# Kernel tuning notes

Hardware: AMD Instinct MI355X
Metric: run time of the kernel (lower is better)

The kernel has to match this reference:

```python
import jax, jax.numpy as jnp
import numpy as np

N_NODES = 100000
N_EDGES = 800000
# (in_dim, out_channels_per_head, heads) for the 5 stacked GATConv layers
DIMS = [(32, 24, 10), (240, 24, 5), (120, 24, 2), (48, 24, 1), (24, 12, 1)]
NEG_SLOPE = 0.2  # PyG GATConv default leaky_relu slope


def setup_inputs() -> dict:
    key = jax.random.key(0)
    ks = jax.random.split(key, 4 + 4 * len(DIMS))
    x = jax.random.normal(ks[0], (N_NODES, 32), jnp.float32)
    # edge_index with no self loops (dst = src + nonzero offset mod N),
    # since PyG GATConv removes then re-adds self loops.
    src = jax.random.randint(ks[1], (N_EDGES,), 0, N_NODES)
    off = jax.random.randint(ks[2], (N_EDGES,), 1, N_NODES)
    dst = (src + off) % N_NODES
    edge_index = jnp.stack([src, dst]).astype(jnp.int32)
    edge_attr = jax.random.normal(ks[3], (N_EDGES, 4), jnp.float32)
    inp = {"x": x, "edge_index": edge_index, "edge_attr": edge_attr}
    for i, (din, c, h) in enumerate(DIMS):
        kw, kb, ka, kd = ks[4 + 4 * i: 8 + 4 * i]
        s = 1.0 / np.sqrt(din)
        inp[f"W{i}"] = jax.random.normal(kw, (din, h * c), jnp.float32) * s
        inp[f"b{i}"] = jax.random.normal(kb, (h * c,), jnp.float32) * 0.01
        inp[f"as{i}"] = jax.random.normal(ka, (h, c), jnp.float32) * (1.0 / np.sqrt(c))
        inp[f"ad{i}"] = jax.random.normal(kd, (h, c), jnp.float32) * (1.0 / np.sqrt(c))
    return inp


def gat_layer(x, src, dst, W, b, a_src, a_dst):
    # Faithful PyG GATConv (concat=True, bias=True, edge_dim=None)
    n = x.shape[0]
    h_heads, c = a_src.shape
    h = (x @ W).reshape(n, h_heads, c)                      # [N,H,C]
    alpha_s = jnp.einsum('nhc,hc->nh', h, a_src)            # [N,H]
    alpha_d = jnp.einsum('nhc,hc->nh', h, a_dst)            # [N,H]
    e = jax.nn.leaky_relu(alpha_s[src] + alpha_d[dst], NEG_SLOPE)  # [E,H]
    # segment softmax over incoming edges of each destination node
    m = jax.ops.segment_max(e, dst, num_segments=n)         # [N,H]
    ex = jnp.exp(e - m[dst])
    z = jax.ops.segment_sum(ex, dst, num_segments=n)        # [N,H]
    attn = ex / z[dst]                                      # [E,H]
    out = jax.ops.segment_sum(h[src] * attn[:, :, None], dst, num_segments=n)
    return out.reshape(n, h_heads * c) + b


def reference(x, edge_index, edge_attr,
              W0, b0, as0, ad0, W1, b1, as1, ad1, W2, b2, as2, ad2,
              W3, b3, as3, ad3, W4, b4, as4, ad4):
    # edge_attr is ignored: GATConv(edge_dim=None) does not use it.
    n = x.shape[0]
    loop = jnp.arange(n, dtype=edge_index.dtype)
    src = jnp.concatenate([edge_index[0], loop])  # add self loops (PyG default)
    dst = jnp.concatenate([edge_index[1], loop])
    params = [(W0, b0, as0, ad0), (W1, b1, as1, ad1), (W2, b2, as2, ad2),
              (W3, b3, as3, ad3), (W4, b4, as4, ad4)]
    for W, b, a_s, a_d in params:
        x = jax.nn.relu(gat_layer(x, src, dst, W, b, a_s, a_d))
    return x
```

## Files before the change

### kernel.cpp

```cpp
#include <hip/hip_runtime.h>
#include <math.h>

#define NN 100000
#define EE 800000
#define ET (EE + NN)
#define BS 256
#define BKTS 391
#define FB_EPB 4096
#define LDSCAP 4096

typedef _Float16 f16;
typedef __attribute__((ext_vector_type(4))) _Float16 half4;
typedef __attribute__((ext_vector_type(8))) _Float16 half8;
typedef __attribute__((ext_vector_type(4))) float f32x4;
template<int V> struct HV;
template<> struct HV<4>{ typedef half4 type; };
template<> struct HV<8>{ typedef half8 type; };

static inline int cdiv(long a, int b){ return (int)((a + b - 1) / b); }

__global__ __launch_bounds__(256) void k_bhist(const int* __restrict__ ei,
                                               int* __restrict__ bucketCount){
    __shared__ int hist[BKTS];
    for (int t = threadIdx.x; t < BKTS; t += 256) hist[t] = 0;
    __syncthreads();
    const int e0 = blockIdx.x * FB_EPB + threadIdx.x;
    #pragma unroll
    for (int i = 0; i < 16; i++){
        int e = e0 + i * 256;
        if (e < ET){
            int d = (e < EE) ? ei[EE + e] : (e - EE);
            atomicAdd(&hist[d >> 8], 1);
        }
    }
    __syncthreads();
    for (int t = threadIdx.x; t < BKTS; t += 256){
        int c = hist[t];
        if (c) atomicAdd(&bucketCount[t], c);
    }
}

__global__ void k_bscan(const int* __restrict__ bucketCount, int* __restrict__ bucketBase,
                        int* __restrict__ bucketCursor, int* __restrict__ rowptr){
    __shared__ int sh[512];
    int t = threadIdx.x;
    int c = (t < BKTS) ? bucketCount[t] : 0;
    sh[t] = c;
    __syncthreads();
    for (int o = 1; o < 512; o <<= 1){
        int v = (t >= o) ? sh[t - o] : 0;
        __syncthreads();
        sh[t] += v;
        __syncthreads();
    }
    if (t < BKTS){
        int excl = sh[t] - c;
        bucketBase[t] = excl;
        bucketCursor[t] = excl;
    }
    if (t == 0){
        bucketBase[BKTS] = ET;
        rowptr[NN] = ET;
    }
}

__global__ __launch_bounds__(256) void k_bfill(const int* __restrict__ ei,
        int* __restrict__ bucketCursor, unsigned* __restrict__ bpack){
    __shared__ int hist[BKTS];
    __shared__ int base[BKTS];
    for (int t = threadIdx.x; t < BKTS; t += 256) hist[t] = 0;
    __syncthreads();
    const int e0 = blockIdx.x * FB_EPB + threadIdx.x;
    unsigned pk[16], rb[16];
    #pragma unroll
    for (int i = 0; i < 16; i++){
        int e = e0 + i * 256;
        rb[i] = 0xFFFFFFFFu;
        if (e < ET){
            int s, d;
            if (e < EE){ s = ei[e]; d = ei[EE + e]; } else { s = e - EE; d = s; }
            int b = d >> 8;
            int r = atomicAdd(&hist[b], 1);
            pk[i] = ((unsigned)(d & 255) << 17) | (unsigned)s;
            rb[i] = ((unsigned)r << 9) | (unsigned)b;
        }
    }
    __syncthreads();
    for (int t = threadIdx.x; t < BKTS; t += 256){
        int c = hist[t];
        base[t] = c ? atomicAdd(&bucketCursor[t], c) : 0;
    }
    __syncthreads();
    #pragma unroll
    for (int i = 0; i < 16; i++){
        if (rb[i] != 0xFFFFFFFFu){
            int b = rb[i] & 511;
            int r = rb[i] >> 9;
            bpack[base[b] + r] = pk[i];
        }
    }
}

__global__ __launch_bounds__(256) void k_bsort(const unsigned* __restrict__ bpack,
        const int* __restrict__ bucketBase, int* __restrict__ rowptr,
        int* __restrict__ ssrc, int* __restrict__ sdst){
    __shared__ int cnt[256];
    __shared__ int off[256];
    __shared__ unsigned stage[LDSCAP];
    int b = blockIdx.x;
    int n0 = bucketBase[b], n1 = bucketBase[b + 1];
    int nE = n1 - n0;
    int t = threadIdx.x;
    cnt[t] = 0;
    __syncthreads();
    for (int i = t; i < nE; i += 256){
        unsigned v = bpack[n0 + i];
        atomicAdd(&cnt[v >> 17], 1);
    }
    __syncthreads();
    int cv = cnt[t];
    off[t] = cv;
    __syncthreads();
    for (int o = 1; o < 256; o <<= 1){
        int v = (t >= o) ? off[t - o] : 0;
        __syncthreads();
        off[t] += v;
        __syncthreads();
    }
    int excl = off[t] - cv;
    __syncthreads();
    off[t] = excl;
    cnt[t] = 0;
    __syncthreads();
    for (int i = t; i < nE; i += 256){
        unsigned v = bpack[n0 + i];
        int dl = v >> 17;
        int r = atomicAdd(&cnt[dl], 1);
        stage[off[dl] + r] = v;
    }
    int d = b * 256 + t;
    if (d < NN) rowptr[d] = n0 + excl;
    __syncthreads();
    for (int i = t; i < nE; i += 256){
        unsigned v = stage[i];
        ssrc[n0 + i] = (int)(v & 0x1FFFFu);
        sdst[n0 + i] = b * 256 + (int)(v >> 17);
    }
}

template<int K, int M, int KP, int MP, int HH, int CC>
__device__ __forceinline__ void prep_one(int idx, const float* __restrict__ W,
        const float* __restrict__ b, const float* __restrict__ as_,
        const float* __restrict__ ad_, f16* __restrict__ Wpk,
        float* __restrict__ bp, float* __restrict__ Was, float* __restrict__ Wad){
    constexpr int NT = MP / 16;
    if (idx < KP * MP){
        int j    = idx & 7;
        int lane = (idx >> 3) & 63;
        int rest = idx >> 9;
        int nt   = rest % NT;
        int ks   = rest / NT;
        int k = ks * 32 + ((lane >> 4) & 3) * 8 + j;
        int n = nt * 16 + (lane & 15);
        Wpk[idx] = (k < K && n < M) ? (f16)W[k * M + n] : (f16)0.f;
    }
    if (idx < MP) bp[idx] = (idx < M) ? b[idx] : 0.f;
    if (idx < K * HH){
        int k = idx / HH, hd = idx - k * HH;
        float s = 0.f, d = 0.f;
        #pragma unroll
        for (int c = 0; c < CC; c++){
            float w = W[k * M + hd * CC + c];
            s = fmaf(w, as_[hd * CC + c], s);
            d = fmaf(w, ad_[hd * CC + c], d);
        }
        Was[idx] = s;
        Wad[idx] = d;
    }
}

__device__ __forceinline__ void prep_w0(int idx, const float* __restrict__ W0,
                                        f16* __restrict__ Wpk0){
    int j    = idx & 7;
    int lane = (idx >> 3) & 63;
    int nt   = (idx >> 9) & 1;
    int hd   = idx >> 10;
    int k    = ((lane >> 4) & 3) * 8 + j;
    int cih  = nt * 16 + (lane & 15);
    Wpk0[idx] = (cih < 24) ? (f16)W0[k * 240 + hd * 24 + cih] : (f16)0.f;
}

struct PrepAll {
    const float *W[5], *b[5], *as[5], *ad[5];
    f16*   Wpk[5];
    f16*   Wpk0;
    float* bp[5];
    float* Was[5];
    float* Wad[5];
    int*   bucketCount;
};

__global__ void k_prep_all(PrepAll a){
    int idx = blockIdx.x * 256 + threadIdx.x;
    if (idx < 7680)
        prep_one< 32, 240,  32, 240, 10, 24>(idx,         a.W[0], a.b[0], a.as[0], a.ad[0], a.Wpk[0], a.bp[0], a.Was[0], a.Wad[0]);
    else if (idx < 40448)
        prep_one<240, 120, 256, 128,  5, 24>(idx - 7680,  a.W[1], a.b[1], a.as[1], a.ad[1], a.Wpk[1], a.bp[1], a.Was[1], a.Wad[1]);
    else if (idx < 48640)
        prep_one<120,  48, 128,  64,  2, 24>(idx - 40448, a.W[2], a.b[2], a.as[2], a.ad[2], a.Wpk[2], a.bp[2], a.Was[2], a.Wad[2]);
    else if (idx < 50688)
        prep_one< 48,  24,  64,  32,  1, 24>(idx - 48640, a.W[3], a.b[3], a.as[3], a.ad[3], a.Wpk[3], a.bp[3], a.Was[3], a.Wad[3]);
    else if (idx < 51200)
        prep_one< 24,  12,  32,  16,  1, 12>(idx - 50688, a.W[4], a.b[4], a.as[4], a.ad[4], a.Wpk[4], a.bp[4], a.Was[4], a.Wad[4]);
    else if (idx < 61440)
        prep_w0(idx - 51200, a.W[0], a.Wpk0);
    else if (idx < 61440 + BKTS)
        a.bucketCount[idx - 61440] = 0;
}

__global__ void k_cvt_alpha0(const float* __restrict__ X, f16* __restrict__ Xh,
                             const float* __restrict__ Was, const float* __restrict__ Wad,
                             float* __restrict__ als, float* __restrict__ ald){
    int n = blockIdx.x * BS + threadIdx.x;
    if (n >= NN) return;
    float xr[32];
    #pragma unroll
    for (int i = 0; i < 8; i++){
        float4 v = *(const float4*)(X + (long)n * 32 + i * 4);
        xr[i * 4 + 0] = v.x; xr[i * 4 + 1] = v.y;
        xr[i * 4 + 2] = v.z; xr[i * 4 + 3] = v.w;
    }
    #pragma unroll
    for (int i = 0; i < 4; i++){
        half8 h;
        #pragma unroll
        for (int c = 0; c < 8; c++) h[c] = (f16)xr[i * 8 + c];
        *(half8*)(Xh + (long)n * 32 + i * 8) = h;
    }
    float s[10] = {}, d[10] = {};
    for (int k = 0; k < 32; k++){
        float x = xr[k];
        #pragma unroll
        for (int hd = 0; hd < 10; hd++){
            s[hd] = fmaf(x, Was[k * 10 + hd], s[hd]);
            d[hd] = fmaf(x, Wad[k * 10 + hd], d[hd]);
        }
    }
    #pragma unroll
    for (int hd = 0; hd < 10; hd++){
        als[n * 10 + hd] = s[hd];
        ald[n * 10 + hd] = d[hd];
    }
}

template<int MPH, int HH, int CC>
__global__ void k_alpha_h(const f16* __restrict__ H2, const float* __restrict__ as_,
                          const float* __restrict__ ad_, float* __restrict__ als,
                          float* __restrict__ ald){
    int n = blockIdx.x * BS + threadIdx.x;
    if (n >= NN) return;
    const f16* h = H2 + (long)n * MPH;
    #pragma unroll
    for (int hd = 0; hd < HH; hd++){
        float s = 0.f, d = 0.f;
        #pragma unroll
        for (int c0 = 0; c0 < CC; c0 += 4){
            half4 hv = *(const half4*)(h + hd * CC + c0);
            #pragma unroll
            for (int j = 0; j < 4; j++){
                float hvf = (float)hv[j];
                s = fmaf(hvf, as_[hd * CC + c0 + j], s);
                d = fmaf(hvf, ad_[hd * CC + c0 + j], d);
            }
        }
        als[n * HH + hd] = s;
        ald[n * HH + hd] = d;
    }
}

template<int HH>
__global__ void k_mz2(const float* __restrict__ als, const float* __restrict__ ald,
                      const int* __restrict__ rowptr, const int* __restrict__ ssrc,
                      float* __restrict__ marr, float* __restrict__ zinvarr){
    int idx = blockIdx.x * BS + threadIdx.x;
    if (idx >= NN * HH) return;
    int n = idx / HH, hd = idx - n * HH;
    float adv = ald[idx];
    int beg = rowptr[n], end = rowptr[n + 1];
    float ma = -1e30f;
    for (int p = beg; p < end; p++)
        ma = fmaxf(ma, als[ssrc[p] * HH + hd]);
    float m = ma + adv;
    m = (m >= 0.f) ? m : 0.2f * m;
    float z = 0.f;
    for (int p = beg; p < end; p++){
        float e = als[ssrc[p] * HH + hd] + adv;
        e = (e >= 0.f) ? e : 0.2f * e;
        z += __expf(e - m);
    }
    marr[idx] = m;
    zinvarr[idx] = 1.f / z;
}

template<int HH, int ATTS, bool GROUPED>
__global__ __launch_bounds__(256) void k_att_edge(const float* __restrict__ als,
        const float* __restrict__ ald, const float* __restrict__ marr,
        const float* __restrict__ zinv, const int* __restrict__ ssrc,
        const int* __restrict__ sdst, f16* __restrict__ att){
    int p = blockIdx.x * 256 + threadIdx.x;
    if (p >= ET) return;
    int s = ssrc[p], d = sdst[p];
    float w[HH];
    #pragma unroll
    for (int hd = 0; hd < HH; hd++){
        float e = als[s * HH + hd] + ald[d * HH + hd];
        e = (e >= 0.f) ? e : 0.2f * e;
        w[hd] = __expf(e - marr[d * HH + hd]) * zinv[d * HH + hd];
    }
    if constexpr (GROUPED){
        half8 lo = {}, hi = {};
        #pragma unroll
        for (int h = 0; h < 5; h++){ lo[h] = (f16)w[h]; hi[h] = (f16)w[h + 5]; }
        *(half8*)(att + (long)p * 16)     = lo;
        *(half8*)(att + (long)p * 16 + 8) = hi;
    } else {
        half8 v = {};
        #pragma unroll
        for (int h = 0; h < HH; h++) v[h] = (f16)w[h];
        *(half8*)(att + (long)p * ATTS) = v;
    }
}

template<int HH, int ATTS>
__global__ void k_mz_att(const float* __restrict__ als, const float* __restrict__ ald,
                         const int* __restrict__ rowptr, const int* __restrict__ ssrc,
                         f16* __restrict__ att){
    int idx = blockIdx.x * BS + threadIdx.x;
    if (idx >= NN * HH) return;
    int n = idx / HH, hd = idx - n * HH;
    float adv = ald[idx];
    int beg = rowptr[n], end = rowptr[n + 1];
    float ma = -1e30f;
    for (int p = beg; p < end; p++)
        ma = fmaxf(ma, als[ssrc[p] * HH + hd]);
    float m = ma + adv;
    m = (m >= 0.f) ? m : 0.2f * m;
    float z = 0.f;
    for (int p = beg; p < end; p++){
        float e = als[ssrc[p] * HH + hd] + adv;
        e = (e >= 0.f) ? e : 0.2f * e;
        z += __expf(e - m);
    }
    float zinv = 1.f / z;
    for (int p = beg; p < end; p++){
        float e = als[ssrc[p] * HH + hd] + adv;
        e = (e >= 0.f) ? e : 0.2f * e;
        att[(long)p * ATTS + hd] = (f16)(__expf(e - m) * zinv);
    }
}

__global__ __launch_bounds__(256) void k_aggX0(const f16* __restrict__ Xh,
        const f16* __restrict__ att, const int* __restrict__ rowptr,
        const int* __restrict__ ssrc, f16* __restrict__ Xagg){
    int idx = blockIdx.x * 256 + threadIdx.x;
    if (idx >= NN * 8) return;
    int n = idx >> 3;
    int hg = (idx >> 2) & 1;
    int ch = idx & 3;
    float acc[5][8] = {};
    int beg = rowptr[n], end = rowptr[n + 1];
    int p = beg;
    for (; p + 2 <= end; p += 2){
        int s0 = ssrc[p], s1 = ssrc[p + 1];
        half8 x0 = *(const half8*)(Xh + (long)s0 * 32 + ch * 8);
        half8 x1 = *(const half8*)(Xh + (long)s1 * 32 + ch * 8);
        half8 a0 = *(const half8*)(att + (long)p * 16 + hg * 8);
        half8 a1 = *(const half8*)(att + (long)(p + 1) * 16 + hg * 8);
        #pragma unroll
        for (int h = 0; h < 5; h++){
            float w0 = (float)a0[h], w1 = (float)a1[h];
            #pragma unroll
            for (int c = 0; c < 8; c++){
                acc[h][c] = fmaf(w0, (float)x0[c], acc[h][c]);
                acc[h][c] = fmaf(w1, (float)x1[c], acc[h][c]);
            }
        }
    }
    if (p < end){
        int s = ssrc[p];
        half8 xv = *(const half8*)(Xh + (long)s * 32 + ch * 8);
        half8 av = *(const half8*)(att + (long)p * 16 + hg * 8);
        #pragma unroll
        for (int h = 0; h < 5; h++){
            float w = (float)av[h];
            #pragma unroll
            for (int c = 0; c < 8; c++)
                acc[h][c] = fmaf(w, (float)xv[c], acc[h][c]);
        }
    }
    #pragma unroll
    for (int h = 0; h < 5; h++){
        half8 o;
        #pragma unroll
        for (int c = 0; c < 8; c++) o[c] = (f16)acc[h][c];
        *(half8*)(Xagg + (long)n * 320 + (hg * 5 + h) * 32 + ch * 8) = o;
    }
}

__global__ __launch_bounds__(256) void k_gemmX0(const f16* __restrict__ Xagg,
        const f16* __restrict__ Wpk0, const float* __restrict__ bp0,
        f16* __restrict__ X1){
    const int wave = threadIdx.x >> 6;
    const int lane = threadIdx.x & 63;
    const int quad = lane >> 4;
    const int l16  = lane & 15;
    const int hd   = blockIdx.y;
    const long row0 = (long)blockIdx.x * 128 + wave * 32;
    const long r0 = row0 + l16;
    const long r1 = r0 + 16;
    const half8 hz = {};
    half8 a0 = (r0 < NN) ? *(const half8*)(Xagg + r0 * 320 + hd * 32 + quad * 8) : hz;
    half8 a1 = (r1 < NN) ? *(const half8*)(Xagg + r1 * 320 + hd * 32 + quad * 8) : hz;
    f32x4 acc[2][2];
    #pragma unroll
    for (int mt = 0; mt < 2; mt++)
        #pragma unroll
        for (int nt = 0; nt < 2; nt++)
            acc[mt][nt] = (f32x4){0.f, 0.f, 0.f, 0.f};
    #pragma unroll
    for (int nt = 0; nt < 2; nt++){
        half8 bfr = *(const half8*)(Wpk0 + ((hd * 2 + nt) * 64 + lane) * 8);
        acc[0][nt] = __builtin_amdgcn_mfma_f32_16x16x32_f16(a0, bfr, acc[0][nt], 0, 0, 0);
        acc[1][nt] = __builtin_amdgcn_mfma_f32_16x16x32_f16(a1, bfr, acc[1][nt], 0, 0, 0);
    }
    #pragma unroll
    for (int mt = 0; mt < 2; mt++){
        #pragma unroll
        for (int reg = 0; reg < 4; reg++){
            long r = row0 + mt * 16 + quad * 4 + reg;
            if (r < NN){
                #pragma unroll
                for (int nt = 0; nt < 2; nt++){
                    int cih = nt * 16 + l16;
                    if (cih < 24){
                        int j = hd * 24 + cih;
                        float v = acc[mt][nt][reg] + bp0[j];
                        X1[r * 256 + j] = (f16)((v > 0.f) ? v : 0.f);
                    }
                }
            }
        }
    }
}

template<int KP, int MPH>
__global__ __launch_bounds__(256) void k_gemm_mfma(const f16* __restrict__ Xh,
        const f16* __restrict__ Wpk, f16* __restrict__ H2){
    constexpr int NT = MPH / 16;
    constexpr int KS = KP / 32;
    const int wave = threadIdx.x >> 6;
    const int lane = threadIdx.x & 63;
    const int quad = lane >> 4;
    const int l16  = lane & 15;
    const long row0 = (long)blockIdx.x * 128 + wave * 32;

    f32x4 acc[2][NT];
    #pragma unroll
    for (int mt = 0; mt < 2; mt++)
        #pragma unroll
        for (int nt = 0; nt < NT; nt++)
            acc[mt][nt] = (f32x4){0.f, 0.f, 0.f, 0.f};

    const long r0 = row0 + l16;
    const long r1 = row0 + 16 + l16;
    const half8 hz = {};
    half8 a0 = (r0 < NN) ? *(const half8*)(Xh + r0 * KP + quad * 8) : hz;
    half8 a1 = (r1 < NN) ? *(const half8*)(Xh + r1 * KP + quad * 8) : hz;
    half8 bc[NT];
    #pragma unroll
    for (int nt = 0; nt < NT; nt++)
        bc[nt] = *(const half8*)(Wpk + ((long)nt * 64 + lane) * 8);

    for (int ks = 0; ks < KS; ks++){
        half8 n0 = hz, n1 = hz, bn[NT];
        if (ks + 1 < KS){
            const int kk = (ks + 1) * 32 + quad * 8;
            n0 = (r0 < NN) ? *(const half8*)(Xh + r0 * KP + kk) : hz;
            n1 = (r1 < NN) ? *(const half8*)(Xh + r1 * KP + kk) : hz;
            const f16* bp_ = Wpk + ((long)(ks + 1) * NT * 64 + lane) * 8;
            #pragma unroll
            for (int nt = 0; nt < NT; nt++)
                bn[nt] = *(const half8*)(bp_ + (long)nt * 512);
        } else {
            #pragma unroll
            for (int nt = 0; nt < NT; nt++) bn[nt] = hz;
        }
        #pragma unroll
        for (int nt = 0; nt < NT; nt++){
            acc[0][nt] = __builtin_amdgcn_mfma_f32_16x16x32_f16(a0, bc[nt], acc[0][nt], 0, 0, 0);
            acc[1][nt] = __builtin_amdgcn_mfma_f32_16x16x32_f16(a1, bc[nt], acc[1][nt], 0, 0, 0);
        }
        a0 = n0; a1 = n1;
        #pragma unroll
        for (int nt = 0; nt < NT; nt++) bc[nt] = bn[nt];
    }
    #pragma unroll
    for (int mt = 0; mt < 2; mt++){
        #pragma unroll
        for (int reg = 0; reg < 4; reg++){
            long r = row0 + mt * 16 + quad * 4 + reg;
            if (r < NN){
                #pragma unroll
                for (int nt = 0; nt < NT; nt++)
                    H2[r * MPH + nt * 16 + l16] = (f16)acc[mt][nt][reg];
            }
        }
    }
}

template<int HH, int CC, int ATTS, int MPH, int MPO, int VEC, bool O16>
__global__ __launch_bounds__(256) void k_agg_h(const f16* __restrict__ H2,
        const f16* __restrict__ att,
        const int* __restrict__ rowptr, const int* __restrict__ ssrc,
        const float* __restrict__ bp, f16* __restrict__ out16,
        float* __restrict__ out32, int MREAL){
    constexpr int TPN = MPO / VEC;
    typedef typename HV<VEC>::type hvec;
    int idx = blockIdx.x * 256 + threadIdx.x;
    if (idx >= NN * TPN) return;
    int n = idx / TPN;
    int q = idx - n * TPN;
    int j0 = q * VEC;
    if constexpr (O16 && (MPO > MPH)){
        if (j0 >= MPH){
            hvec zv = {};
            *(hvec*)(out16 + (long)n * MPO + j0) = zv;
            return;
        }
    }
    int hd = j0 / CC; if (hd > HH - 1) hd = HH - 1;

    int beg = rowptr[n], end = rowptr[n + 1];
    float acc[VEC] = {};
    int p = beg;
    for (; p + 2 <= end; p += 2){
        int s0 = ssrc[p], s1 = ssrc[p + 1];
        float w0 = (float)att[(long)p * ATTS + hd];
        float w1 = (float)att[(long)(p + 1) * ATTS + hd];
        hvec h0 = *(const hvec*)(H2 + (long)s0 * MPH + j0);
        hvec h1 = *(const hvec*)(H2 + (long)s1 * MPH + j0);
        #pragma unroll
        for (int c = 0; c < VEC; c++){
            acc[c] = fmaf(w0, (float)h0[c], acc[c]);
            acc[c] = fmaf(w1, (float)h1[c], acc[c]);
        }
    }
    if (p < end){
        int s = ssrc[p];
        float w = (float)att[(long)p * ATTS + hd];
        hvec hv = *(const hvec*)(H2 + (long)s * MPH + j0);
        #pragma unroll
        for (int c = 0; c < VEC; c++)
            acc[c] = fmaf(w, (float)hv[c], acc[c]);
    }
    if constexpr (O16){
        hvec o;
        #pragma unroll
        for (int c = 0; c < VEC; c++){
            float v = acc[c] + bp[j0 + c];
            o[c] = (f16)((v > 0.f) ? v : 0.f);
        }
        *(hvec*)(out16 + (long)n * MPO + j0) = o;
    } else {
        if (j0 < MREAL){
            #pragma unroll
            for (int c = 0; c < VEC; c++){
                float v = acc[c] + bp[j0 + c];
                out32[(long)n * MREAL + j0 + c] = (v > 0.f) ? v : 0.f;
            }
        }
    }
}

template<int K, int M, int KP, int MPH, int MPO, int HH, int CC, int ATTS, int VEC,
         bool O16, bool EDGEATT>
static void run_layer(const f16* Xh, f16* H2, f16* att,
                      const f16* Wpk, const float* bp,
                      const float* asv, const float* adv,
                      float* als, float* ald, float* marr, float* zinv,
                      const int* rowptr, const int* ssrc, const int* sdst,
                      f16* Xnext, float* out32, hipStream_t stream){
    constexpr int TPN = MPO / VEC;
    k_gemm_mfma<KP, MPH><<<cdiv(NN, 128), 256, 0, stream>>>(Xh, Wpk, H2);
    k_alpha_h<MPH, HH, CC><<<cdiv(NN, BS), BS, 0, stream>>>(H2, asv, adv, als, ald);
    if constexpr (EDGEATT){
        k_mz2<HH><<<cdiv((long)NN * HH, BS), BS, 0, stream>>>(als, ald, rowptr, ssrc, marr, zinv);
        k_att_edge<HH, ATTS, false><<<cdiv(ET, 256), 256, 0, stream>>>(
            als, ald, marr, zinv, ssrc, sdst, att);
    } else {
        k_mz_att<HH, ATTS><<<cdiv((long)NN * HH, BS), BS, 0, stream>>>(
            als, ald, rowptr, ssrc, att);
    }
    k_agg_h<HH, CC, ATTS, MPH, MPO, VEC, O16><<<cdiv((long)NN * TPN, 256), 256, 0, stream>>>(
        H2, att, rowptr, ssrc, bp, Xnext, out32, M);
}

extern "C" void kernel_launch(void* const* d_in, const int* in_sizes, int n_in,
                              void* d_out, int out_size, void* d_ws, size_t ws_size,
                              hipStream_t stream){
    const float* x0 = (const float*)d_in[0];
    const int*   ei = (const int*)d_in[1];
    PrepAll pa;
    for (int i = 0; i < 5; i++){
        pa.W[i]  = (const float*)d_in[3 + 4 * i];
        pa.b[i]  = (const float*)d_in[4 + 4 * i];
        pa.as[i] = (const float*)d_in[5 + 4 * i];
        pa.ad[i] = (const float*)d_in[6 + 4 * i];
    }

    char* p = (char*)d_ws;
    auto alloc = [&](size_t bytes) -> char* {
        char* r = p;
        p += (bytes + 255) & ~(size_t)255;
        return r;
    };
    f16*   Xh     = (f16*)alloc((size_t)NN * 256 * 2);
    f16*   H2     = (f16*)alloc((size_t)NN * 320 * 2);
    f16*   att    = (f16*)alloc((size_t)ET * 16 * 2);
    float* als    = (float*)alloc((size_t)NN * 10 * 4);
    float* ald    = (float*)alloc((size_t)NN * 10 * 4);
    float* marr   = (float*)alloc((size_t)NN * 10 * 4);
    float* zinv   = (float*)alloc((size_t)NN * 10 * 4);
    const int wpkSz[5] = {7680, 32768, 8192, 2048, 512};
    const int mpSz[5]  = {240, 128, 64, 32, 16};
    const int khSz[5]  = {320, 1200, 240, 48, 24};
    for (int i = 0; i < 5; i++){
        pa.Wpk[i] = (f16*)alloc((size_t)wpkSz[i] * 2);
        pa.bp[i]  = (float*)alloc((size_t)mpSz[i] * 4);
        pa.Was[i] = (float*)alloc((size_t)khSz[i] * 4);
        pa.Wad[i] = (float*)alloc((size_t)khSz[i] * 4);
    }
    pa.Wpk0 = (f16*)alloc((size_t)10240 * 2);
    int*      bucketCount  = (int*)alloc((size_t)BKTS * 4);
    int*      bucketBase   = (int*)alloc((size_t)(BKTS + 1) * 4);
    int*      bucketCursor = (int*)alloc((size_t)BKTS * 4);
    unsigned* bpack        = (unsigned*)alloc((size_t)ET * 4);
    int*      rowptr       = (int*)alloc((size_t)(NN + 1) * 4);
    int*      ssrc         = (int*)alloc((size_t)ET * 4);
    int*      sdst         = (int*)alloc((size_t)ET * 4);
    pa.bucketCount = bucketCount;

    k_prep_all<<<242, 256, 0, stream>>>(pa);
    k_bhist<<<cdiv(ET, FB_EPB), 256, 0, stream>>>(ei, bucketCount);
    k_bscan<<<1, 512, 0, stream>>>(bucketCount, bucketBase, bucketCursor, rowptr);
    k_bfill<<<cdiv(ET, FB_EPB), 256, 0, stream>>>(ei, bucketCursor, bpack);
    k_bsort<<<BKTS, 256, 0, stream>>>(bpack, bucketBase, rowptr, ssrc, sdst);

    k_cvt_alpha0<<<cdiv(NN, BS), BS, 0, stream>>>(x0, Xh, pa.Was[0], pa.Wad[0], als, ald);
    k_mz2<10><<<cdiv((long)NN * 10, BS), BS, 0, stream>>>(als, ald, rowptr, ssrc, marr, zinv);
    k_att_edge<10, 16, true><<<cdiv(ET, 256), 256, 0, stream>>>(
        als, ald, marr, zinv, ssrc, sdst, att);
    k_aggX0<<<cdiv((long)NN * 8, 256), 256, 0, stream>>>(Xh, att, rowptr, ssrc, H2 );
    dim3 g0(cdiv(NN, 128), 10);
    k_gemmX0<<<g0, 256, 0, stream>>>(H2 , pa.Wpk0, pa.bp[0], Xh );

    run_layer<240, 120, 256, 128, 128,  5, 24, 8, 8, true,  true >(Xh, H2, att, pa.Wpk[1],
        pa.bp[1], pa.as[1], pa.ad[1], als, ald, marr, zinv, rowptr, ssrc, sdst, Xh, nullptr, stream);
    run_layer<120,  48, 128,  64,  64,  2, 24, 2, 8, true,  false>(Xh, H2, att, pa.Wpk[2],
        pa.bp[2], pa.as[2], pa.ad[2], als, ald, marr, zinv, rowptr, ssrc, sdst, Xh, nullptr, stream);
    run_layer< 48,  24,  64,  32,  32,  1, 24, 1, 8, true,  false>(Xh, H2, att, pa.Wpk[3],
        pa.bp[3], pa.as[3], pa.ad[3], als, ald, marr, zinv, rowptr, ssrc, sdst, Xh, nullptr, stream);
    run_layer< 24,  12,  32,  16,  16,  1, 12, 1, 4, false, false>(Xh, H2, att, pa.Wpk[4],
        pa.bp[4], pa.as[4], pa.ad[4], als, ald, marr, zinv, rowptr, ssrc, sdst, nullptr, (float*)d_out, stream);
}
```

Before: 527.7 us.

## Fuse layer-0 aggregation with per-head projection through shared memory

Merges the layer-0 aggregate-then-transform step (aggregation kernel plus MFMA GEMM kernel) into one kernel. Aggregated 320-wide rows go into LDS and are multiplied there by a plain row-major fp16 copy of W0 using scalar FMAs, which removes the global round trip of the intermediate buffer and one launch. The cost is replacing MFMA with scalar FMA work, about 18KB of LDS per block that may limit occupancy, and separate buffers for layer-0 input and layer-1+ activations.

```diff
diff --git a/kernel.cpp b/kernel.cpp
--- a/kernel.cpp
+++ b/kernel.cpp
@@ -179,21 +179,10 @@
     }
 }
 
-__device__ __forceinline__ void prep_w0(int idx, const float* __restrict__ W0,
-                                        f16* __restrict__ Wpk0){
-    int j    = idx & 7;
-    int lane = (idx >> 3) & 63;
-    int nt   = (idx >> 9) & 1;
-    int hd   = idx >> 10;
-    int k    = ((lane >> 4) & 3) * 8 + j;
-    int cih  = nt * 16 + (lane & 15);
-    Wpk0[idx] = (cih < 24) ? (f16)W0[k * 240 + hd * 24 + cih] : (f16)0.f;
-}
-
 struct PrepAll {
     const float *W[5], *b[5], *as[5], *ad[5];
     f16*   Wpk[5];
-    f16*   Wpk0;
+    f16*   W0h;
     float* bp[5];
     float* Was[5];
     float* Wad[5];
@@ -212,8 +201,13 @@
         prep_one< 48,  24,  64,  32,  1, 24>(idx - 48640, a.W[3], a.b[3], a.as[3], a.ad[3], a.Wpk[3], a.bp[3], a.Was[3], a.Wad[3]);
     else if (idx < 51200)
         prep_one< 24,  12,  32,  16,  1, 12>(idx - 50688, a.W[4], a.b[4], a.as[4], a.ad[4], a.Wpk[4], a.bp[4], a.Was[4], a.Wad[4]);
-    else if (idx < 61440)
-        prep_w0(idx - 51200, a.W[0], a.Wpk0);
+    else if (idx < 61440){
+        int i2 = idx - 51200;
+        int hd = i2 >> 10;
+        int k  = (i2 >> 5) & 31;
+        int c  = i2 & 31;
+        a.W0h[i2] = (c < 24) ? (f16)a.W[0][k * 240 + hd * 24 + c] : (f16)0.f;
+    }
     else if (idx < 61440 + BKTS)
         a.bucketCount[idx - 61440] = 0;
 }
@@ -359,97 +353,88 @@
     }
 }
 
-__global__ __launch_bounds__(256) void k_aggX0(const f16* __restrict__ Xh,
+__global__ __launch_bounds__(256) void k_aggX0f(const f16* __restrict__ Xh,
         const f16* __restrict__ att, const int* __restrict__ rowptr,
-        const int* __restrict__ ssrc, f16* __restrict__ Xagg){
-    int idx = blockIdx.x * 256 + threadIdx.x;
-    if (idx >= NN * 8) return;
-    int n = idx >> 3;
-    int hg = (idx >> 2) & 1;
-    int ch = idx & 3;
+        const int* __restrict__ ssrc, const f16* __restrict__ W0h,
+        const float* __restrict__ bp0, f16* __restrict__ X1){
+    __shared__ f16 xs[32 * 336];
+    const int tid = threadIdx.x;
+    const int nl = tid >> 3;
+    const long n = (long)blockIdx.x * 32 + nl;
+    const int hg = (tid >> 2) & 1;
+    const int ch = tid & 3;
     float acc[5][8] = {};
-    int beg = rowptr[n], end = rowptr[n + 1];
-    int p = beg;
-    for (; p + 2 <= end; p += 2){
-        int s0 = ssrc[p], s1 = ssrc[p + 1];
-        half8 x0 = *(const half8*)(Xh + (long)s0 * 32 + ch * 8);
-        half8 x1 = *(const half8*)(Xh + (long)s1 * 32 + ch * 8);
-        half8 a0 = *(const half8*)(att + (long)p * 16 + hg * 8);
-        half8 a1 = *(const half8*)(att + (long)(p + 1) * 16 + hg * 8);
-        #pragma unroll
-        for (int h = 0; h < 5; h++){
-            float w0 = (float)a0[h], w1 = (float)a1[h];
+    if (n < NN){
+        int beg = rowptr[n], end = rowptr[n + 1];
+        int p = beg;
+        for (; p + 2 <= end; p += 2){
+            int s0 = ssrc[p], s1 = ssrc[p + 1];
+            half8 x0 = *(const half8*)(Xh + (long)s0 * 32 + ch * 8);
+            half8 x1 = *(const half8*)(Xh + (long)s1 * 32 + ch * 8);
+            half8 a0 = *(const half8*)(att + (long)p * 16 + hg * 8);
+            half8 a1 = *(const half8*)(att + (long)(p + 1) * 16 + hg * 8);
             #pragma unroll
-            for (int c = 0; c < 8; c++){
-                acc[h][c] = fmaf(w0, (float)x0[c], acc[h][c]);
-                acc[h][c] = fmaf(w1, (float)x1[c], acc[h][c]);
+            for (int h = 0; h < 5; h++){
+                float w0 = (float)a0[h], w1 = (float)a1[h];
+                #pragma unroll
+                for (int c = 0; c < 8; c++){
+                    acc[h][c] = fmaf(w0, (float)x0[c], acc[h][c]);
+                    acc[h][c] = fmaf(w1, (float)x1[c], acc[h][c]);
+                }
             }
         }
-    }
-    if (p < end){
-        int s = ssrc[p];
-        half8 xv = *(const half8*)(Xh + (long)s * 32 + ch * 8);
-        half8 av = *(const half8*)(att + (long)p * 16 + hg * 8);
-        #pragma unroll
-        for (int h = 0; h < 5; h++){
-            float w = (float)av[h];
+        if (p < end){
+            int s = ssrc[p];
+            half8 xv = *(const half8*)(Xh + (long)s * 32 + ch * 8);
+            half8 av = *(const half8*)(att + (long)p * 16 + hg * 8);
+            #pragma unroll
+            for (int h = 0; h < 5; h++){
+                float w = (float)av[h];
+                #pragma unroll
+                for (int c = 0; c < 8; c++)
+                    acc[h][c] = fmaf(w, (float)xv[c], acc[h][c]);
+            }
+        }
+    }
+    #pragma unroll
+    for (int h = 0; h < 5; h++){
+        half8 o;
+        #pragma unroll
+        for (int c = 0; c < 8; c++) o[c] = (f16)acc[h][c];
+        *(half8*)(xs + nl * 336 + (hg * 5 + h) * 32 + ch * 8) = o;
+    }
+    __syncthreads();
+    #pragma unroll
+    for (int it = 0; it < 4; it++){
+        int cidx = tid + it * 256;
+        int onl = cidx >> 5;
+        int oc  = (cidx & 31) * 8;
+        long on = (long)blockIdx.x * 32 + onl;
+        if (on >= NN) continue;
+        if (oc >= 240){
+            half8 z = {};
+            *(half8*)(X1 + on * 256 + oc) = z;
+            continue;
+        }
+        int hd = oc / 24;
+        int c0 = oc - hd * 24;
+        float o[8];
+        #pragma unroll
+        for (int c = 0; c < 8; c++) o[c] = bp0[oc + c];
+        const f16* xrow = xs + onl * 336 + hd * 32;
+        const f16* wrow = W0h + (long)hd * 1024 + c0;
+        #pragma unroll 4
+        for (int k = 0; k < 32; k++){
+            float x = (float)xrow[k];
+            half8 wv = *(const half8*)(wrow + k * 32);
             #pragma unroll
             for (int c = 0; c < 8; c++)
-                acc[h][c] = fmaf(w, (float)xv[c], acc[h][c]);
-        }
-    }
-    #pragma unroll
-    for (int h = 0; h < 5; h++){
-        half8 o;
-        #pragma unroll
-        for (int c = 0; c < 8; c++) o[c] = (f16)acc[h][c];
-        *(half8*)(Xagg + (long)n * 320 + (hg * 5 + h) * 32 + ch * 8) = o;
-    }
-}
-
-__global__ __launch_bounds__(256) void k_gemmX0(const f16* __restrict__ Xagg,
-        const f16* __restrict__ Wpk0, const float* __restrict__ bp0,
-        f16* __restrict__ X1){
-    const int wave = threadIdx.x >> 6;
-    const int lane = threadIdx.x & 63;
-    const int quad = lane >> 4;
-    const int l16  = lane & 15;
-    const int hd   = blockIdx.y;
-    const long row0 = (long)blockIdx.x * 128 + wave * 32;
-    const long r0 = row0 + l16;
-    const long r1 = r0 + 16;
-    const half8 hz = {};
-    half8 a0 = (r0 < NN) ? *(const half8*)(Xagg + r0 * 320 + hd * 32 + quad * 8) : hz;
-    half8 a1 = (r1 < NN) ? *(const half8*)(Xagg + r1 * 320 + hd * 32 + quad * 8) : hz;
-    f32x4 acc[2][2];
-    #pragma unroll
-    for (int mt = 0; mt < 2; mt++)
-        #pragma unroll
-        for (int nt = 0; nt < 2; nt++)
-            acc[mt][nt] = (f32x4){0.f, 0.f, 0.f, 0.f};
-    #pragma unroll
-    for (int nt = 0; nt < 2; nt++){
-        half8 bfr = *(const half8*)(Wpk0 + ((hd * 2 + nt) * 64 + lane) * 8);
-        acc[0][nt] = __builtin_amdgcn_mfma_f32_16x16x32_f16(a0, bfr, acc[0][nt], 0, 0, 0);
-        acc[1][nt] = __builtin_amdgcn_mfma_f32_16x16x32_f16(a1, bfr, acc[1][nt], 0, 0, 0);
-    }
-    #pragma unroll
-    for (int mt = 0; mt < 2; mt++){
-        #pragma unroll
-        for (int reg = 0; reg < 4; reg++){
-            long r = row0 + mt * 16 + quad * 4 + reg;
-            if (r < NN){
-                #pragma unroll
-                for (int nt = 0; nt < 2; nt++){
-                    int cih = nt * 16 + l16;
-                    if (cih < 24){
-                        int j = hd * 24 + cih;
-                        float v = acc[mt][nt][reg] + bp0[j];
-                        X1[r * 256 + j] = (f16)((v > 0.f) ? v : 0.f);
-                    }
-                }
-            }
-        }
+                o[c] = fmaf(x, (float)wv[c], o[c]);
+        }
+        half8 ov;
+        #pragma unroll
+        for (int c = 0; c < 8; c++) ov[c] = (f16)((o[c] > 0.f) ? o[c] : 0.f);
+        *(half8*)(X1 + on * 256 + oc) = ov;
     }
 }
 
@@ -624,8 +609,9 @@
         p += (bytes + 255) & ~(size_t)255;
         return r;
     };
-    f16*   Xh     = (f16*)alloc((size_t)NN * 256 * 2);
-    f16*   H2     = (f16*)alloc((size_t)NN * 320 * 2);
+    f16*   Xh     = (f16*)alloc((size_t)NN * 32 * 2);
+    f16*   Xb     = (f16*)alloc((size_t)NN * 256 * 2);
+    f16*   H2     = (f16*)alloc((size_t)NN * 128 * 2);
     f16*   att    = (f16*)alloc((size_t)ET * 16 * 2);
     float* als    = (float*)alloc((size_t)NN * 10 * 4);
     float* ald    = (float*)alloc((size_t)NN * 10 * 4);
@@ -640,7 +626,7 @@
         pa.Was[i] = (float*)alloc((size_t)khSz[i] * 4);
         pa.Wad[i] = (float*)alloc((size_t)khSz[i] * 4);
     }
-    pa.Wpk0 = (f16*)alloc((size_t)10240 * 2);
+    pa.W0h = (f16*)alloc((size_t)10240 * 2);
     int*      bucketCount  = (int*)alloc((size_t)BKTS * 4);
     int*      bucketBase   = (int*)alloc((size_t)(BKTS + 1) * 4);
     int*      bucketCursor = (int*)alloc((size_t)BKTS * 4);
@@ -660,16 +646,15 @@
     k_mz2<10><<<cdiv((long)NN * 10, BS), BS, 0, stream>>>(als, ald, rowptr, ssrc, marr, zinv);
     k_att_edge<10, 16, true><<<cdiv(ET, 256), 256, 0, stream>>>(
         als, ald, marr, zinv, ssrc, sdst, att);
-    k_aggX0<<<cdiv((long)NN * 8, 256), 256, 0, stream>>>(Xh, att, rowptr, ssrc, H2 );
-    dim3 g0(cdiv(NN, 128), 10);
-    k_gemmX0<<<g0, 256, 0, stream>>>(H2 , pa.Wpk0, pa.bp[0], Xh );
-
-    run_layer<240, 120, 256, 128, 128,  5, 24, 8, 8, true,  true >(Xh, H2, att, pa.Wpk[1],
-        pa.bp[1], pa.as[1], pa.ad[1], als, ald, marr, zinv, rowptr, ssrc, sdst, Xh, nullptr, stream);
-    run_layer<120,  48, 128,  64,  64,  2, 24, 2, 8, true,  false>(Xh, H2, att, pa.Wpk[2],
-        pa.bp[2], pa.as[2], pa.ad[2], als, ald, marr, zinv, rowptr, ssrc, sdst, Xh, nullptr, stream);
-    run_layer< 48,  24,  64,  32,  32,  1, 24, 1, 8, true,  false>(Xh, H2, att, pa.Wpk[3],
-        pa.bp[3], pa.as[3], pa.ad[3], als, ald, marr, zinv, rowptr, ssrc, sdst, Xh, nullptr, stream);
-    run_layer< 24,  12,  32,  16,  16,  1, 12, 1, 4, false, false>(Xh, H2, att, pa.Wpk[4],
+    k_aggX0f<<<cdiv(NN, 32), 256, 0, stream>>>(Xh, att, rowptr, ssrc, pa.W0h,
+                                               pa.bp[0], Xb );
+
+    run_layer<240, 120, 256, 128, 128,  5, 24, 8, 8, true,  true >(Xb, H2, att, pa.Wpk[1],
+        pa.bp[1], pa.as[1], pa.ad[1], als, ald, marr, zinv, rowptr, ssrc, sdst, Xb, nullptr, stream);
+    run_layer<120,  48, 128,  64,  64,  2, 24, 2, 8, true,  false>(Xb, H2, att, pa.Wpk[2],
+        pa.bp[2], pa.as[2], pa.ad[2], als, ald, marr, zinv, rowptr, ssrc, sdst, Xb, nullptr, stream);
+    run_layer< 48,  24,  64,  32,  32,  1, 24, 1, 8, true,  false>(Xb, H2, att, pa.Wpk[3],
+        pa.bp[3], pa.as[3], pa.ad[3], als, ald, marr, zinv, rowptr, ssrc, sdst, Xb, nullptr, stream);
+    run_layer< 24,  12,  32,  16,  16,  1, 12, 1, 4, false, false>(Xb, H2, att, pa.Wpk[4],
         pa.bp[4], pa.as[4], pa.ad[4], als, ald, marr, zinv, rowptr, ssrc, sdst, nullptr, (float*)d_out, stream);
 }
```

Measured after the change: 569.6 us. 7.9% more time.
